# Kernel tuning notes

Hardware: AMD Instinct MI355X
Metric: run time of the kernel (lower is better)

## Reference

```python
import jax, jax.numpy as jnp
import numpy as np

B, N, F = 32, 64, 128

def mish(x):
    return x * jnp.tanh(jax.nn.softplus(x))

def residual_mlp(x, W1, b1, W2, b2):
    # ResidualModule(simple_mlp(d, d, d)): x + Linear2(mish(Linear1(x)))
    h = mish(x @ W1 + b1)
    return x + (h @ W2 + b2)

def setup_inputs() -> dict:
    key = jax.random.key(0)
    ks = jax.random.split(key, 20)
    inp = {
        'embeddings': jax.random.normal(ks[0], (B * N, F), dtype=jnp.float32),
        'num_objects': jnp.full((B,), N, dtype=jnp.int64 if jax.config.jax_enable_x64 else jnp.int32),
    }
    i = 1
    # arity-1 predicate p0: width F; arity-2 predicates p1..p3: width 2F
    for name, d in [('p0', F), ('p1', 2 * F), ('p2', 2 * F), ('p3', 2 * F)]:
        inp[f'W1_{name}'] = jax.random.normal(ks[i], (d, d), dtype=jnp.float32) * 0.05; i += 1
        inp[f'b1_{name}'] = jnp.zeros((d,), dtype=jnp.float32)
        inp[f'W2_{name}'] = jax.random.normal(ks[i], (d, d), dtype=jnp.float32) * 0.05; i += 1
        inp[f'b2_{name}'] = jnp.zeros((d,), dtype=jnp.float32)
    return inp

def reference(embeddings, num_objects,
              W1_p0, b1_p0, W2_p0, b2_p0,
              W1_p1, b1_p1, W2_p1, b2_p1,
              W1_p2, b1_p2, W2_p2, b2_p2,
              W1_p3, b1_p3, W2_p3, b2_p3):
    b = num_objects.shape[0]
    n = embeddings.shape[0] // b          # uniform object count per state
    f = embeddings.shape[1]
    x = embeddings.reshape(b, n, f)       # per-state object embeddings
    # arity 1: every object is a length-1 permutation -> rows are embeddings themselves
    rows_a1 = embeddings                  # [b*n, f]
    # arity 2: all ordered pairs (product with replacement) -> concat features
    left = jnp.broadcast_to(x[:, :, None, :], (b, n, n, f))
    right = jnp.broadcast_to(x[:, None, :, :], (b, n, n, f))
    rows_a2 = jnp.concatenate([left, right], axis=-1).reshape(b * n * n, 2 * f)
    out_p0 = residual_mlp(rows_a1, W1_p0, b1_p0, W2_p0, b2_p0)
    out_p1 = residual_mlp(rows_a2, W1_p1, b1_p1, W2_p1, b2_p1)
    out_p2 = residual_mlp(rows_a2, W1_p2, b1_p2, W2_p2, b2_p2)
    out_p3 = residual_mlp(rows_a2, W1_p3, b1_p3, W2_p3, b2_p3)
    return (out_p0, out_p1, out_p2, out_p3)
```

## Files before the change

### kernel.cpp

```cpp
#include <hip/hip_runtime.h>

typedef __bf16 bf16;
typedef bf16 bf16x8 __attribute__((ext_vector_type(8)));
typedef float floatx4 __attribute__((ext_vector_type(4)));

__device__ __forceinline__ float mish_f(float x) {
  float e = __expf(fminf(x, 20.0f));
  float p = 1.0f + e;
  float p2 = p * p;
  return x * (p2 - 1.0f) * __builtin_amdgcn_rcpf(p2 + 1.0f);
}

struct PrepArgs {
  const float* emb;
  const float* W[8];
  bf16* emb_bf;
  bf16* Wp[8];
};

__global__ __launch_bounds__(256) void prep_kernel(PrepArgs a) {
  const int idx = blockIdx.x * 256 + threadIdx.x;
  const int EMB_N = 2048 * 128;
  if (idx < EMB_N) {
    a.emb_bf[idx] = (bf16)a.emb[idx];
    return;
  }
  int t = idx - EMB_N;
  int m, local, D, lognct;
  if (t < 32768) {
    m = t >> 14; local = t & 16383; D = 128; lognct = 3;
  } else {
    int u = t - 32768;
    m = 2 + (u >> 16); local = u & 65535; D = 256; lognct = 4;
  }
  if (m >= 8) return;
  const int j    = local & 7;
  const int lane = (local >> 3) & 63;
  const int ctk  = local >> 9;
  const int ct   = ctk & ((1 << lognct) - 1);
  const int kt   = ctk >> lognct;
  const int row  = kt * 32 + (lane >> 4) * 8 + j;
  const int col  = ct * 16 + (lane & 15);
  a.Wp[m][local] = (bf16)a.W[m][row * D + col];
}

template <int NCT, int NKT, int STRIDE, int CPW>
__device__ __forceinline__ void gemm_tiles(const bf16* lds_a,
                                           const bf16* __restrict__ Wp,
                                           int w, int lane,
                                           floatx4 acc[4][CPW]) {
  const int l15 = lane & 15;
  const int q   = lane >> 4;
  for (int kt = 0; kt < NKT; ++kt) {
    bf16x8 af[4];
#pragma unroll
    for (int mt = 0; mt < 4; ++mt)
      af[mt] = *(const bf16x8*)&lds_a[(mt * 16 + l15) * STRIDE + kt * 32 + q * 8];
    bf16x8 bfr[CPW];
#pragma unroll
    for (int c = 0; c < CPW; ++c)
      bfr[c] = *(const bf16x8*)(Wp + (((kt * NCT) + (w * CPW + c)) * 64 + lane) * 8);
#pragma unroll
    for (int mt = 0; mt < 4; ++mt)
#pragma unroll
      for (int c = 0; c < CPW; ++c)
        acc[mt][c] = __builtin_amdgcn_mfma_f32_16x16x32_bf16(af[mt], bfr[c], acc[mt][c], 0, 0, 0);
  }
}

struct A2Args {
  const bf16* emb_bf;
  const float* emb_f;
  const bf16* W1p[3];
  const float* b1[3];
  const bf16* W2p[3];
  const float* b2[3];
  float* out[3];
};

__global__ __launch_bounds__(256, 4) void fused_a2(A2Args a) {
  const int p  = blockIdx.y;
  const int r0 = blockIdx.x * 64;
  const int bb = r0 >> 12;
  const int ii = (r0 >> 6) & 63;
  const int t  = threadIdx.x;
  const int lane = t & 63;
  const int w    = t >> 6;
  const int l15  = lane & 15;
  const int q    = lane >> 4;

  __shared__ bf16 lds[64 * 264];

  {
    const int row = t >> 2;
    const int qt  = t & 3;
    const bf16* src = (qt < 2)
        ? (a.emb_bf + (bb * 64 + ii) * 128 + qt * 64)
        : (a.emb_bf + (bb * 64 + row) * 128 + (qt - 2) * 64);
    const uint4* s4 = (const uint4*)src;
    uint4* d4 = (uint4*)&lds[row * 264 + qt * 64];
#pragma unroll
    for (int u = 0; u < 8; ++u) d4[u] = s4[u];
  }
  __syncthreads();

  floatx4 acc[4][4];
#pragma unroll
  for (int mt = 0; mt < 4; ++mt)
#pragma unroll
    for (int c = 0; c < 4; ++c) acc[mt][c] = (floatx4){0.f, 0.f, 0.f, 0.f};
  gemm_tiles<16, 8, 264, 4>(lds, a.W1p[p], w, lane, acc);

  float b1v[4];
  {
    const float* b1 = a.b1[p];
#pragma unroll
    for (int c = 0; c < 4; ++c) b1v[c] = b1[w * 64 + c * 16 + l15];
  }

  __syncthreads();
#pragma unroll
  for (int mt = 0; mt < 4; ++mt)
#pragma unroll
    for (int c = 0; c < 4; ++c) {
      const int col = w * 64 + c * 16 + l15;
#pragma unroll
      for (int r = 0; r < 4; ++r) {
        float x = acc[mt][c][r] + b1v[c];
        lds[(mt * 16 + q * 4 + r) * 264 + col] = (bf16)mish_f(x);
      }
    }
  __syncthreads();

#pragma unroll
  for (int mt = 0; mt < 4; ++mt)
#pragma unroll
    for (int c = 0; c < 4; ++c) acc[mt][c] = (floatx4){0.f, 0.f, 0.f, 0.f};
  gemm_tiles<16, 8, 264, 4>(lds, a.W2p[p], w, lane, acc);

  float b2v[4];
  {
    const float* b2 = a.b2[p];
#pragma unroll
    for (int c = 0; c < 4; ++c) b2v[c] = b2[w * 64 + c * 16 + l15];
  }
  const float* embL = a.emb_f + (bb * 64 + ii) * 128;
  const float* embR = a.emb_f + (bb * 64) * 128;
  float* outp = a.out[p] + (size_t)r0 * 256;

  if (w < 2) {
    float resv[4];
#pragma unroll
    for (int c = 0; c < 4; ++c) resv[c] = embL[w * 64 + c * 16 + l15];
#pragma unroll
    for (int mt = 0; mt < 4; ++mt)
#pragma unroll
      for (int c = 0; c < 4; ++c) {
        const int col = w * 64 + c * 16 + l15;
#pragma unroll
        for (int r = 0; r < 4; ++r) {
          const int rl = mt * 16 + q * 4 + r;
          outp[rl * 256 + col] = acc[mt][c][r] + b2v[c] + resv[c];
        }
      }
  } else {
#pragma unroll
    for (int mt = 0; mt < 4; ++mt)
#pragma unroll
      for (int c = 0; c < 4; ++c) {
        const int col = w * 64 + c * 16 + l15;
#pragma unroll
        for (int r = 0; r < 4; ++r) {
          const int rl = mt * 16 + q * 4 + r;
          outp[rl * 256 + col] = acc[mt][c][r] + b2v[c] + embR[rl * 128 + (col - 128)];
        }
      }
  }
}

struct A1Args {
  const bf16* emb_bf;
  const float* emb_f;
  const bf16* W1p;
  const float* b1;
  const bf16* W2p;
  const float* b2;
  float* out;
};

__global__ __launch_bounds__(256, 4) void fused_a1(A1Args a) {
  const int r0 = blockIdx.x * 64;
  const int t  = threadIdx.x;
  const int lane = t & 63;
  const int w    = t >> 6;
  const int l15  = lane & 15;
  const int q    = lane >> 4;

  __shared__ bf16 lds[64 * 136];

  {
    const int row = t >> 2;
    const int qt  = t & 3;
    const bf16* src = a.emb_bf + (r0 + row) * 128 + qt * 32;
    const uint4* s4 = (const uint4*)src;
    uint4* d4 = (uint4*)&lds[row * 136 + qt * 32];
#pragma unroll
    for (int u = 0; u < 4; ++u) d4[u] = s4[u];
  }
  __syncthreads();

  floatx4 acc[4][2];
#pragma unroll
  for (int mt = 0; mt < 4; ++mt)
#pragma unroll
    for (int c = 0; c < 2; ++c) acc[mt][c] = (floatx4){0.f, 0.f, 0.f, 0.f};
  gemm_tiles<8, 4, 136, 2>(lds, a.W1p, w, lane, acc);

  float b1v[2];
#pragma unroll
  for (int c = 0; c < 2; ++c) b1v[c] = a.b1[w * 32 + c * 16 + l15];

  __syncthreads();
#pragma unroll
  for (int mt = 0; mt < 4; ++mt)
#pragma unroll
    for (int c = 0; c < 2; ++c) {
      const int col = w * 32 + c * 16 + l15;
#pragma unroll
      for (int r = 0; r < 4; ++r) {
        float x = acc[mt][c][r] + b1v[c];
        lds[(mt * 16 + q * 4 + r) * 136 + col] = (bf16)mish_f(x);
      }
    }
  __syncthreads();

#pragma unroll
  for (int mt = 0; mt < 4; ++mt)
#pragma unroll
    for (int c = 0; c < 2; ++c) acc[mt][c] = (floatx4){0.f, 0.f, 0.f, 0.f};
  gemm_tiles<8, 4, 136, 2>(lds, a.W2p, w, lane, acc);

  float b2v[2];
#pragma unroll
  for (int c = 0; c < 2; ++c) b2v[c] = a.b2[w * 32 + c * 16 + l15];

#pragma unroll
  for (int mt = 0; mt < 4; ++mt)
#pragma unroll
    for (int c = 0; c < 2; ++c) {
      const int col = w * 32 + c * 16 + l15;
#pragma unroll
      for (int r = 0; r < 4; ++r) {
        const int rl = mt * 16 + q * 4 + r;
        a.out[(r0 + rl) * 128 + col] =
            acc[mt][c][r] + b2v[c] + a.emb_f[(r0 + rl) * 128 + col];
      }
    }
}

extern "C" void kernel_launch(void* const* d_in, const int* in_sizes, int n_in,
                              void* d_out, int out_size, void* d_ws, size_t ws_size,
                              hipStream_t stream) {
  const float* emb_f = (const float*)d_in[0];
  const float* W1s[4], *b1s[4], *W2s[4], *b2s[4];
  for (int p = 0; p < 4; ++p) {
    W1s[p] = (const float*)d_in[2 + p * 4 + 0];
    b1s[p] = (const float*)d_in[2 + p * 4 + 1];
    W2s[p] = (const float*)d_in[2 + p * 4 + 2];
    b2s[p] = (const float*)d_in[2 + p * 4 + 3];
  }

  char* ws = (char*)d_ws;
  bf16* emb_bf = (bf16*)ws;
  size_t off = (size_t)2048 * 128 * 2;
  bf16* Wp[8];
  const size_t wbytes[8] = {32768, 32768, 131072, 131072, 131072, 131072, 131072, 131072};
  for (int m = 0; m < 8; ++m) { Wp[m] = (bf16*)(ws + off); off += wbytes[m]; }

  PrepArgs pa;
  pa.emb = emb_f;
  pa.emb_bf = emb_bf;
  const float* Wsrc[8] = {W1s[0], W2s[0], W1s[1], W2s[1], W1s[2], W2s[2], W1s[3], W2s[3]};
  for (int m = 0; m < 8; ++m) { pa.W[m] = Wsrc[m]; pa.Wp[m] = Wp[m]; }
  prep_kernel<<<2688, 256, 0, stream>>>(pa);

  float* out = (float*)d_out;

  A1Args a1;
  a1.emb_bf = emb_bf; a1.emb_f = emb_f;
  a1.W1p = Wp[0]; a1.b1 = b1s[0]; a1.W2p = Wp[1]; a1.b2 = b2s[0];
  a1.out = out;
  fused_a1<<<32, 256, 0, stream>>>(a1);

  A2Args a2;
  a2.emb_bf = emb_bf; a2.emb_f = emb_f;
  size_t o = 2048 * 128;
  for (int p = 0; p < 3; ++p) {
    a2.W1p[p] = Wp[2 + p * 2];
    a2.W2p[p] = Wp[3 + p * 2];
    a2.b1[p] = b1s[p + 1];
    a2.b2[p] = b2s[p + 1];
    a2.out[p] = out + o + (size_t)p * 131072 * 256;
  }
  fused_a2<<<dim3(2048, 3), 256, 0, stream>>>(a2);
}
```

Measured before the change: 566.7 us.

## Factor first-layer GEMM of pair MLPs into per-object U and V projections

Because each pair row is a concat of two object embeddings, x@W1 splits into the left object times the top half of W1 plus the right object times the bottom half. A new kernel computes these per-object projections U (with bias) and V once for all 2048 objects. The pair kernel then only adds U and V, applies mish, and runs the second GEMM, which removes half of its matrix work. The pair outputs are also written with nontemporal stores. In exchange it adds an extra launch, fp32 U/V buffers in workspace, and bf16 rounding at a different point.

```diff
diff --git a/kernel.cpp b/kernel.cpp
--- a/kernel.cpp
+++ b/kernel.cpp
@@ -2,6 +2,7 @@
 
 typedef __bf16 bf16;
 typedef bf16 bf16x8 __attribute__((ext_vector_type(8)));
+typedef bf16 bf16x4 __attribute__((ext_vector_type(4)));
 typedef float floatx4 __attribute__((ext_vector_type(4)));
 
 __device__ __forceinline__ float mish_f(float x) {
@@ -68,11 +69,84 @@
   }
 }
 
-struct A2Args {
+struct UVArgs {
   const bf16* emb_bf;
-  const float* emb_f;
   const bf16* W1p[3];
   const float* b1[3];
+  float* U[3];
+  float* V[3];
+};
+
+__global__ __launch_bounds__(256) void uv_kernel(UVArgs a) {
+  const int p  = blockIdx.y;
+  const int r0 = blockIdx.x * 64;
+  const int t  = threadIdx.x;
+  const int lane = t & 63;
+  const int w    = t >> 6;
+  const int l15  = lane & 15;
+  const int q    = lane >> 4;
+
+  __shared__ bf16 lds[64 * 136];
+
+  {
+    const int row = t >> 2;
+    const int qt  = t & 3;
+    const uint4* s4 = (const uint4*)(a.emb_bf + (r0 + row) * 128 + qt * 32);
+    uint4* d4 = (uint4*)&lds[row * 136 + qt * 32];
+#pragma unroll
+    for (int u = 0; u < 4; ++u) d4[u] = s4[u];
+  }
+  __syncthreads();
+
+  floatx4 acc[4][4];
+
+#pragma unroll
+  for (int mt = 0; mt < 4; ++mt)
+#pragma unroll
+    for (int c = 0; c < 4; ++c) acc[mt][c] = (floatx4){0.f, 0.f, 0.f, 0.f};
+  gemm_tiles<16, 4, 136, 4>(lds, a.W1p[p], w, lane, acc);
+
+  float b1v[4];
+#pragma unroll
+  for (int c = 0; c < 4; ++c) b1v[c] = a.b1[p][w * 64 + c * 16 + l15];
+
+  float* Up = a.U[p] + (size_t)r0 * 256;
+#pragma unroll
+  for (int mt = 0; mt < 4; ++mt)
+#pragma unroll
+    for (int c = 0; c < 4; ++c) {
+      const int col = w * 64 + c * 16 + l15;
+#pragma unroll
+      for (int r = 0; r < 4; ++r) {
+        const int rl = mt * 16 + q * 4 + r;
+        Up[rl * 256 + col] = acc[mt][c][r] + b1v[c];
+      }
+    }
+
+#pragma unroll
+  for (int mt = 0; mt < 4; ++mt)
+#pragma unroll
+    for (int c = 0; c < 4; ++c) acc[mt][c] = (floatx4){0.f, 0.f, 0.f, 0.f};
+  gemm_tiles<16, 4, 136, 4>(lds, a.W1p[p] + 32768, w, lane, acc);
+
+  float* Vp = a.V[p] + (size_t)r0 * 256;
+#pragma unroll
+  for (int mt = 0; mt < 4; ++mt)
+#pragma unroll
+    for (int c = 0; c < 4; ++c) {
+      const int col = w * 64 + c * 16 + l15;
+#pragma unroll
+      for (int r = 0; r < 4; ++r) {
+        const int rl = mt * 16 + q * 4 + r;
+        Vp[rl * 256 + col] = acc[mt][c][r];
+      }
+    }
+}
+
+struct A2Args {
+  const float* U[3];
+  const float* V[3];
+  const float* emb_f;
   const bf16* W2p[3];
   const float* b2[3];
   float* out[3];
@@ -92,46 +166,24 @@
   __shared__ bf16 lds[64 * 264];
 
   {
-    const int row = t >> 2;
-    const int qt  = t & 3;
-    const bf16* src = (qt < 2)
-        ? (a.emb_bf + (bb * 64 + ii) * 128 + qt * 64)
-        : (a.emb_bf + (bb * 64 + row) * 128 + (qt - 2) * 64);
-    const uint4* s4 = (const uint4*)src;
-    uint4* d4 = (uint4*)&lds[row * 264 + qt * 64];
-#pragma unroll
-    for (int u = 0; u < 8; ++u) d4[u] = s4[u];
+    const int col4 = t & 63;
+    const int wq   = t >> 6;
+    const floatx4 uvv =
+        ((const floatx4*)(a.U[p] + (size_t)(bb * 64 + ii) * 256))[col4];
+    const float* Vblk = a.V[p] + (size_t)(bb * 64) * 256;
+#pragma unroll
+    for (int r = 0; r < 16; ++r) {
+      const int row = wq * 16 + r;
+      const floatx4 v = ((const floatx4*)(Vblk + row * 256))[col4];
+      bf16x4 hv;
+#pragma unroll
+      for (int e = 0; e < 4; ++e) hv[e] = (bf16)mish_f(uvv[e] + v[e]);
+      *(bf16x4*)&lds[row * 264 + col4 * 4] = hv;
+    }
   }
   __syncthreads();
 
   floatx4 acc[4][4];
-#pragma unroll
-  for (int mt = 0; mt < 4; ++mt)
-#pragma unroll
-    for (int c = 0; c < 4; ++c) acc[mt][c] = (floatx4){0.f, 0.f, 0.f, 0.f};
-  gemm_tiles<16, 8, 264, 4>(lds, a.W1p[p], w, lane, acc);
-
-  float b1v[4];
-  {
-    const float* b1 = a.b1[p];
-#pragma unroll
-    for (int c = 0; c < 4; ++c) b1v[c] = b1[w * 64 + c * 16 + l15];
-  }
-
-  __syncthreads();
-#pragma unroll
-  for (int mt = 0; mt < 4; ++mt)
-#pragma unroll
-    for (int c = 0; c < 4; ++c) {
-      const int col = w * 64 + c * 16 + l15;
-#pragma unroll
-      for (int r = 0; r < 4; ++r) {
-        float x = acc[mt][c][r] + b1v[c];
-        lds[(mt * 16 + q * 4 + r) * 264 + col] = (bf16)mish_f(x);
-      }
-    }
-  __syncthreads();
-
 #pragma unroll
   for (int mt = 0; mt < 4; ++mt)
 #pragma unroll
@@ -144,8 +196,8 @@
 #pragma unroll
     for (int c = 0; c < 4; ++c) b2v[c] = b2[w * 64 + c * 16 + l15];
   }
-  const float* embL = a.emb_f + (bb * 64 + ii) * 128;
-  const float* embR = a.emb_f + (bb * 64) * 128;
+  const float* embL = a.emb_f + (size_t)(bb * 64 + ii) * 128;
+  const float* embR = a.emb_f + (size_t)(bb * 64) * 128;
   float* outp = a.out[p] + (size_t)r0 * 256;
 
   if (w < 2) {
@@ -160,7 +212,8 @@
 #pragma unroll
         for (int r = 0; r < 4; ++r) {
           const int rl = mt * 16 + q * 4 + r;
-          outp[rl * 256 + col] = acc[mt][c][r] + b2v[c] + resv[c];
+          __builtin_nontemporal_store(acc[mt][c][r] + b2v[c] + resv[c],
+                                      &outp[rl * 256 + col]);
         }
       }
   } else {
@@ -172,7 +225,9 @@
 #pragma unroll
         for (int r = 0; r < 4; ++r) {
           const int rl = mt * 16 + q * 4 + r;
-          outp[rl * 256 + col] = acc[mt][c][r] + b2v[c] + embR[rl * 128 + (col - 128)];
+          __builtin_nontemporal_store(
+              acc[mt][c][r] + b2v[c] + embR[rl * 128 + (col - 128)],
+              &outp[rl * 256 + col]);
         }
       }
   }
@@ -276,6 +331,12 @@
   bf16* Wp[8];
   const size_t wbytes[8] = {32768, 32768, 131072, 131072, 131072, 131072, 131072, 131072};
   for (int m = 0; m < 8; ++m) { Wp[m] = (bf16*)(ws + off); off += wbytes[m]; }
+  float* Ub[3];
+  float* Vb[3];
+  for (int p = 0; p < 3; ++p) {
+    Ub[p] = (float*)(ws + off) + (size_t)p * 2 * 2048 * 256;
+    Vb[p] = Ub[p] + (size_t)2048 * 256;
+  }
 
   PrepArgs pa;
   pa.emb = emb_f;
@@ -284,6 +345,16 @@
   for (int m = 0; m < 8; ++m) { pa.W[m] = Wsrc[m]; pa.Wp[m] = Wp[m]; }
   prep_kernel<<<2688, 256, 0, stream>>>(pa);
 
+  UVArgs uva;
+  uva.emb_bf = emb_bf;
+  for (int p = 0; p < 3; ++p) {
+    uva.W1p[p] = Wp[2 + p * 2];
+    uva.b1[p]  = b1s[p + 1];
+    uva.U[p]   = Ub[p];
+    uva.V[p]   = Vb[p];
+  }
+  uv_kernel<<<dim3(32, 3), 256, 0, stream>>>(uva);
+
   float* out = (float*)d_out;
 
   A1Args a1;
@@ -293,12 +364,12 @@
   fused_a1<<<32, 256, 0, stream>>>(a1);
 
   A2Args a2;
-  a2.emb_bf = emb_bf; a2.emb_f = emb_f;
+  a2.emb_f = emb_f;
   size_t o = 2048 * 128;
   for (int p = 0; p < 3; ++p) {
-    a2.W1p[p] = Wp[2 + p * 2];
+    a2.U[p] = Ub[p];
+    a2.V[p] = Vb[p];
     a2.W2p[p] = Wp[3 + p * 2];
-    a2.b1[p] = b1s[p + 1];
     a2.b2[p] = b2s[p + 1];
     a2.out[p] = out + o + (size_t)p * 131072 * 256;
   }
```

Result: faster. 508.5 us (-10.3%).
